# Optimization experiments

Hardware: AMD Instinct MI355X
Metric: run time of the kernel (lower is better)

## Reference

```python
import jax, jax.numpy as jnp
import numpy as np

K = 1024  # num_codebook_vectors
D = 256   # latent_dim


def setup_inputs() -> dict:
    key = jax.random.key(0)
    k1, k2 = jax.random.split(key)
    z = jax.random.normal(k1, (16, D, 64, 64), dtype=jnp.float32)
    # nn.Embedding weight init: uniform(-1/K, 1/K)
    emb_weight = jax.random.uniform(k2, (K, D), dtype=jnp.float32,
                                    minval=-1.0 / K, maxval=1.0 / K)
    return {"z": z, "emb_weight": emb_weight}


def reference(z, emb_weight):
    B, C, H, W = z.shape  # C == D
    # NCHW -> NHWC, flatten to [N, D]
    z_nhwc = jnp.transpose(z, (0, 2, 3, 1))
    zf = z_nhwc.reshape(-1, C)  # [N, D]
    # squared L2 distances: ||z||^2 + ||e||^2 - 2 z e^T
    d = (jnp.sum(zf * zf, axis=1, keepdims=True)
         + jnp.sum(emb_weight * emb_weight, axis=1)
         - 2.0 * jnp.einsum('nd,kd->nk', zf, emb_weight))  # [N, K]
    min_encoding_indices = jnp.argmin(d, axis=1)  # [N] int
    z_q = emb_weight[min_encoding_indices].reshape(B, H, W, C)
    z_q = jnp.transpose(z_q, (0, 3, 1, 2))  # back to NCHW
    return (min_encoding_indices, z_q)
```

## Files before the change

kernel.cpp:

```cpp
#include <hip/hip_runtime.h>
#include <hip/hip_bf16.h>
#include <stdint.h>
#include <stddef.h>

typedef __attribute__((ext_vector_type(4))) float f32x4;
typedef _Float16 f16x8 __attribute__((ext_vector_type(8)));
typedef _Float16 f16x4 __attribute__((ext_vector_type(4)));

#define BN 128
#define MARGIN 230.0f

__device__ float g_embn[1024];

__device__ __forceinline__ int swzA(int n) { return (n ^ (n >> 3)) & 7; }

__global__ __launch_bounds__(256) void emb_prep_kernel(const float* __restrict__ emb,
                                                       _Float16* __restrict__ embf) {
    int row = blockIdx.x * 4 + (threadIdx.x >> 6);
    int l   = threadIdx.x & 63;
    f32x4 v = *(const f32x4*)&emb[(size_t)row * 256 + l * 4];
    f16x4 h;
    float s = 0.f;
#pragma unroll
    for (int j = 0; j < 4; ++j) {
        h[j] = (_Float16)(v[j] * 1024.0f);
        float f = (float)h[j];
        s = fmaf(f, f, s);
    }
    *(f16x4*)&embf[(size_t)row * 256 + l * 4] = h;
#pragma unroll
    for (int off = 1; off < 64; off <<= 1) s += __shfl_xor(s, off, 64);
    if (l == 0) g_embn[row] = s;
}

__device__ __forceinline__ void prefetch_B(const _Float16* __restrict__ embf,
                                           _Float16* bbuf, int s, int t) {
    int kt = s >> 3, ds = s & 7;
    int code = t >> 2;
    int slot = t & 3;
    int g    = (slot ^ code ^ (code >> 2)) & 3;
    const _Float16* src = embf + (((size_t)(kt * 128 + code)) << 8) + ds * 32 + g * 8;
    void* dst = (void*)(bbuf + (size_t)t * 8);
    __builtin_amdgcn_global_load_lds((const __attribute__((address_space(1))) void*)src,
                                     (__attribute__((address_space(3))) void*)dst,
                                     16, 0, 0);
}

__global__ __launch_bounds__(512, 4) void vq_kernel(
        const float* __restrict__ z,
        const float* __restrict__ emb,
        const _Float16* __restrict__ embf,
        float* __restrict__ out) {

    __shared__ _Float16 A_sh[BN * 256];
    __shared__ _Float16 B_sh[2][BN * 32];

    const int t  = threadIdx.x;
    const int w  = t >> 6;
    const int l  = t & 63;
    const int c  = l & 15;
    const int q  = l >> 4;
    const int wr = w >> 1;
    const int wc = w & 1;

    const int n0    = blockIdx.x * BN;
    const int b_img = n0 >> 12;
    const int hw0   = n0 & 4095;
    const float* zb = z + (size_t)b_img * (256 * 4096) + hw0;

    prefetch_B(embf, &B_sh[0][0], 0, t);

#pragma unroll
    for (int it = 0; it < 2; ++it) {
        int task = it * 512 + t;
        int nq = task & 31;
        int dg = task >> 5;
        const float* g = zb + (size_t)(dg * 8) * 4096 + nq * 4;
        f32x4 col[8];
#pragma unroll
        for (int j = 0; j < 8; ++j) col[j] = *(const f32x4*)(g + (size_t)j * 4096);
#pragma unroll
        for (int u = 0; u < 4; ++u) {
            int n = nq * 4 + u;
            f16x8 v;
#pragma unroll
            for (int j = 0; j < 8; ++j) v[j] = (_Float16)col[j][u];
            *(f16x8*)&A_sh[n * 256 + ((dg ^ swzA(n)) * 8)] = v;
        }
    }

    f32x4 acc[2][4];
    float v1[8], v2[8];
    int   i1[8], i2[8];
#pragma unroll
    for (int i = 0; i < 2; ++i)
#pragma unroll
        for (int j = 0; j < 4; ++j) acc[i][j] = (f32x4){0.f, 0.f, 0.f, 0.f};
#pragma unroll
    for (int p = 0; p < 8; ++p) { v1[p] = 3.4e38f; v2[p] = 3.4e38f; i1[p] = 0x7fffffff; i2[p] = 0x7fffffff; }

    for (int kt = 0; kt < 8; ++kt) {
        float en4[4];
#pragma unroll
        for (int j = 0; j < 4; ++j) en4[j] = g_embn[kt * 128 + wc * 64 + j * 16 + c];

#pragma unroll
        for (int ds = 0; ds < 8; ++ds) {
            int s = kt * 8 + ds;
            __syncthreads();
            if (s + 1 < 64) prefetch_B(embf, &B_sh[(s + 1) & 1][0], s + 1, t);

            const _Float16* Bb = &B_sh[s & 1][0];

            f16x8 af[2], bfr[4];
#pragma unroll
            for (int i = 0; i < 2; ++i) {
                int n  = wr * 32 + i * 16 + c;
                int pg = ((ds << 2) + q) ^ swzA(n);
                af[i] = *(const f16x8*)&A_sh[n * 256 + pg * 8];
            }
#pragma unroll
            for (int j = 0; j < 4; ++j) {
                int k = wc * 64 + j * 16 + c;
                bfr[j] = *(const f16x8*)&Bb[k * 32 + (((q ^ k ^ (k >> 2)) & 3) * 8)];
            }
#pragma unroll
            for (int i = 0; i < 2; ++i)
#pragma unroll
                for (int j = 0; j < 4; ++j)
                    acc[i][j] = __builtin_amdgcn_mfma_f32_16x16x32_f16(af[i], bfr[j], acc[i][j], 0, 0, 0);
        }

#pragma unroll
        for (int j = 0; j < 4; ++j) {
            float en = en4[j];
            int code = kt * 128 + wc * 64 + j * 16 + c;
#pragma unroll
            for (int i = 0; i < 2; ++i) {
#pragma unroll
                for (int r = 0; r < 4; ++r) {
                    int p = i * 4 + r;
                    float sc = fmaf(-2048.0f, acc[i][j][r], en);
                    if (sc < v1[p]) {
                        v2[p] = v1[p]; i2[p] = i1[p];
                        v1[p] = sc;    i1[p] = code;
                    } else if (sc < v2[p]) {
                        v2[p] = sc;    i2[p] = code;
                    }
                }
            }
        }
#pragma unroll
        for (int i = 0; i < 2; ++i)
#pragma unroll
            for (int j = 0; j < 4; ++j) acc[i][j] = (f32x4){0.f, 0.f, 0.f, 0.f};
    }

    __syncthreads();

    float* cv = (float*)A_sh;
    int*   ci = ((int*)A_sh) + 8192;
    int* idx_fin = (int*)&B_sh[0][0];
    int* wl_n    = idx_fin + 128;
    int* wl_row  = idx_fin + 129;
    int* wl_nc   = idx_fin + 257;
    int* wl_cand = idx_fin + 385;

    if (t == 0) wl_n[0] = 0;
#pragma unroll
    for (int p = 0; p < 8; ++p) {
        int row = wr * 32 + (p >> 2) * 16 + q * 4 + (p & 3);
        int s0  = (wc * 16 + c) * 2;
        cv[s0 * 128       + ((row + s0)     & 127)] = v1[p];
        ci[s0 * 128       + ((row + s0)     & 127)] = i1[p];
        cv[(s0 + 1) * 128 + ((row + s0 + 1) & 127)] = v2[p];
        ci[(s0 + 1) * 128 + ((row + s0 + 1) & 127)] = i2[p];
    }
    __syncthreads();

    if (t < BN) {
        float mv = 3.4e38f; int mi = 0x7fffffff;
#pragma unroll 8
        for (int s = 0; s < 64; ++s) {
            float v = cv[s * 128 + ((t + s) & 127)];
            int  id = ci[s * 128 + ((t + s) & 127)];
            if (v < mv || (v == mv && id < mi)) { mv = v; mi = id; }
        }
        int   cand[8]; int nc = 0;
        float thr = mv + MARGIN;
        for (int s = 0; s < 64; ++s) {
            float v = cv[s * 128 + ((t + s) & 127)];
            int  id = ci[s * 128 + ((t + s) & 127)];
            if (v <= thr && id < 1024 && nc < 8) cand[nc++] = id;
        }
        idx_fin[t] = mi;
        if (nc > 1) {
            int slot = atomicAdd(wl_n, 1);
            wl_row[slot] = t;
            wl_nc[slot]  = nc;
            for (int i = 0; i < nc; ++i) wl_cand[slot * 8 + i] = cand[i];
        }
    }
    __syncthreads();

    int nwl = wl_n[0];
    for (int e = w; e < nwl; e += 8) {
        int row = wl_row[e];
        int nc  = wl_nc[e];
        const float* zrow = zb + row;

        int j  = l & 15, h = j >> 3, jj = j & 7;
        float x0 = zrow[(size_t)(h * 128 + jj) * 4096];
        float r  = __fmul_rn(x0, x0);
        for (int m = 1; m < 16; ++m) {
            float x = zrow[(size_t)(h * 128 + jj + 8 * m) * 4096];
            r = __fadd_rn(r, __fmul_rn(x, x));
        }
        float s1 = __fadd_rn(r,  __shfl_xor(r,  1, 64));
        float s2 = __fadd_rn(s1, __shfl_xor(s1, 2, 64));
        float s4 = __fadd_rn(s2, __shfl_xor(s2, 4, 64));
        float a_n = __fadd_rn(s4, __shfl_xor(s4, 8, 64));
        a_n = __shfl(a_n, 0, 64);

        float best = 3.4e38f; int bid = 0x7fffffff;
        for (int cx = 0; cx < nc; ++cx) {
            int id = wl_cand[e * 8 + cx];
            const float* er = emb + (size_t)id * 256;
            float y0 = er[h * 128 + jj];
            float rb = __fmul_rn(y0, y0);
            for (int m = 1; m < 16; ++m) {
                float y = er[h * 128 + jj + 8 * m];
                rb = __fadd_rn(rb, __fmul_rn(y, y));
            }
            float b1 = __fadd_rn(rb, __shfl_xor(rb, 1, 64));
            float b2 = __fadd_rn(b1, __shfl_xor(b1, 2, 64));
            float b4 = __fadd_rn(b2, __shfl_xor(b2, 4, 64));
            float b_k = __fadd_rn(b4, __shfl_xor(b4, 8, 64));
            b_k = __shfl(b_k, 0, 64);
            double cd = 0.0;
#pragma unroll
            for (int u = 0; u < 4; ++u) {
                int d = l + u * 64;
                cd = fma((double)zrow[(size_t)d * 4096], (double)er[d], cd);
            }
#pragma unroll
            for (int off = 1; off < 64; off <<= 1) cd += __shfl_xor(cd, off, 64);
            float c32 = (float)cd;
            float sc  = __fsub_rn(__fadd_rn(a_n, b_k), __fmul_rn(2.0f, c32));
            if (sc < best || (sc == best && id < bid)) { best = sc; bid = id; }
        }
        if (l == 0) idx_fin[row] = bid;
    }
    __syncthreads();

    if (t < BN) out[n0 + t] = (float)idx_fin[t];

    float* zq = out + 65536 + (size_t)b_img * (256 * 4096) + hw0;
    {
        int m   = t & 127;
        int sub = t >> 7;
        int id  = idx_fin[m];
        const float* er = emb + (size_t)id * 256;
#pragma unroll 4
        for (int it = 0; it < 16; ++it) {
            int d4 = it * 4 + sub;
            f32x4 v = *(const f32x4*)&er[d4 * 4];
#pragma unroll
            for (int jj2 = 0; jj2 < 4; ++jj2)
                zq[(size_t)(d4 * 4 + jj2) * 4096 + m] = v[jj2];
        }
    }
}

extern "C" void kernel_launch(void* const* d_in, const int* in_sizes, int n_in,
                              void* d_out, int out_size, void* d_ws, size_t ws_size,
                              hipStream_t stream) {
    const float* z   = (const float*)d_in[0];
    const float* emb = (const float*)d_in[1];
    _Float16* embf = (_Float16*)d_ws;
    float* out = (float*)d_out;

    emb_prep_kernel<<<256, 256, 0, stream>>>(emb, embf);
    vq_kernel<<<65536 / BN, 512, 0, stream>>>(z, emb, embf, out);
}
```

Before: 192.0 us.

## Use 1024-thread blocks with 16 waves each computing a 16-row tile

Doubles the block size to 1024 threads so each wave handles 16 rows instead of 32, halving per-wave MFMA work and register state, and spreads the z staging, candidate refinement and gather loops across twice as many threads. The aim is more waves in flight to hide latency. In exchange, each B fragment loaded from LDS now feeds only one A fragment, so LDS read traffic per MFMA rises. The per-step __syncthreads also has to coordinate 16 waves instead of 8.

```diff
diff --git a/kernel.cpp b/kernel.cpp
--- a/kernel.cpp
+++ b/kernel.cpp
@@ -46,7 +46,7 @@
                                      16, 0, 0);
 }
 
-__global__ __launch_bounds__(512, 4) void vq_kernel(
+__global__ __launch_bounds__(1024, 8) void vq_kernel(
         const float* __restrict__ z,
         const float* __restrict__ emb,
         const _Float16* __restrict__ embf,
@@ -68,13 +68,11 @@
     const int hw0   = n0 & 4095;
     const float* zb = z + (size_t)b_img * (256 * 4096) + hw0;
 
-    prefetch_B(embf, &B_sh[0][0], 0, t);
-
-#pragma unroll
-    for (int it = 0; it < 2; ++it) {
-        int task = it * 512 + t;
-        int nq = task & 31;
-        int dg = task >> 5;
+    if (t < 512) prefetch_B(embf, &B_sh[0][0], 0, t);
+
+    {
+        int nq = t & 31;
+        int dg = t >> 5;
         const float* g = zb + (size_t)(dg * 8) * 4096 + nq * 4;
         f32x4 col[8];
 #pragma unroll
@@ -89,15 +87,13 @@
         }
     }
 
-    f32x4 acc[2][4];
-    float v1[8], v2[8];
-    int   i1[8], i2[8];
-#pragma unroll
-    for (int i = 0; i < 2; ++i)
-#pragma unroll
-        for (int j = 0; j < 4; ++j) acc[i][j] = (f32x4){0.f, 0.f, 0.f, 0.f};
-#pragma unroll
-    for (int p = 0; p < 8; ++p) { v1[p] = 3.4e38f; v2[p] = 3.4e38f; i1[p] = 0x7fffffff; i2[p] = 0x7fffffff; }
+    f32x4 acc[4];
+    float v1[4], v2[4];
+    int   i1[4], i2[4];
+#pragma unroll
+    for (int j = 0; j < 4; ++j) acc[j] = (f32x4){0.f, 0.f, 0.f, 0.f};
+#pragma unroll
+    for (int p = 0; p < 4; ++p) { v1[p] = 3.4e38f; v2[p] = 3.4e38f; i1[p] = 0x7fffffff; i2[p] = 0x7fffffff; }
 
     for (int kt = 0; kt < 8; ++kt) {
         float en4[4];
@@ -108,16 +104,15 @@
         for (int ds = 0; ds < 8; ++ds) {
             int s = kt * 8 + ds;
             __syncthreads();
-            if (s + 1 < 64) prefetch_B(embf, &B_sh[(s + 1) & 1][0], s + 1, t);
+            if (s + 1 < 64 && t < 512) prefetch_B(embf, &B_sh[(s + 1) & 1][0], s + 1, t);
 
             const _Float16* Bb = &B_sh[s & 1][0];
 
-            f16x8 af[2], bfr[4];
-#pragma unroll
-            for (int i = 0; i < 2; ++i) {
-                int n  = wr * 32 + i * 16 + c;
+            f16x8 af, bfr[4];
+            {
+                int n  = wr * 16 + c;
                 int pg = ((ds << 2) + q) ^ swzA(n);
-                af[i] = *(const f16x8*)&A_sh[n * 256 + pg * 8];
+                af = *(const f16x8*)&A_sh[n * 256 + pg * 8];
             }
 #pragma unroll
             for (int j = 0; j < 4; ++j) {
@@ -125,10 +120,8 @@
                 bfr[j] = *(const f16x8*)&Bb[k * 32 + (((q ^ k ^ (k >> 2)) & 3) * 8)];
             }
 #pragma unroll
-            for (int i = 0; i < 2; ++i)
-#pragma unroll
-                for (int j = 0; j < 4; ++j)
-                    acc[i][j] = __builtin_amdgcn_mfma_f32_16x16x32_f16(af[i], bfr[j], acc[i][j], 0, 0, 0);
+            for (int j = 0; j < 4; ++j)
+                acc[j] = __builtin_amdgcn_mfma_f32_16x16x32_f16(af, bfr[j], acc[j], 0, 0, 0);
         }
 
 #pragma unroll
@@ -136,24 +129,18 @@
             float en = en4[j];
             int code = kt * 128 + wc * 64 + j * 16 + c;
 #pragma unroll
-            for (int i = 0; i < 2; ++i) {
-#pragma unroll
-                for (int r = 0; r < 4; ++r) {
-                    int p = i * 4 + r;
-                    float sc = fmaf(-2048.0f, acc[i][j][r], en);
-                    if (sc < v1[p]) {
-                        v2[p] = v1[p]; i2[p] = i1[p];
-                        v1[p] = sc;    i1[p] = code;
-                    } else if (sc < v2[p]) {
-                        v2[p] = sc;    i2[p] = code;
-                    }
+            for (int r = 0; r < 4; ++r) {
+                float sc = fmaf(-2048.0f, acc[j][r], en);
+                if (sc < v1[r]) {
+                    v2[r] = v1[r]; i2[r] = i1[r];
+                    v1[r] = sc;    i1[r] = code;
+                } else if (sc < v2[r]) {
+                    v2[r] = sc;    i2[r] = code;
                 }
             }
         }
 #pragma unroll
-        for (int i = 0; i < 2; ++i)
-#pragma unroll
-            for (int j = 0; j < 4; ++j) acc[i][j] = (f32x4){0.f, 0.f, 0.f, 0.f};
+        for (int j = 0; j < 4; ++j) acc[j] = (f32x4){0.f, 0.f, 0.f, 0.f};
     }
 
     __syncthreads();
@@ -168,8 +155,8 @@
 
     if (t == 0) wl_n[0] = 0;
 #pragma unroll
-    for (int p = 0; p < 8; ++p) {
-        int row = wr * 32 + (p >> 2) * 16 + q * 4 + (p & 3);
+    for (int p = 0; p < 4; ++p) {
+        int row = wr * 16 + q * 4 + p;
         int s0  = (wc * 16 + c) * 2;
         cv[s0 * 128       + ((row + s0)     & 127)] = v1[p];
         ci[s0 * 128       + ((row + s0)     & 127)] = i1[p];
@@ -204,7 +191,7 @@
     __syncthreads();
 
     int nwl = wl_n[0];
-    for (int e = w; e < nwl; e += 8) {
+    for (int e = w; e < nwl; e += 16) {
         int row = wl_row[e];
         int nc  = wl_nc[e];
         const float* zrow = zb + row;
@@ -261,9 +248,9 @@
         int sub = t >> 7;
         int id  = idx_fin[m];
         const float* er = emb + (size_t)id * 256;
-#pragma unroll 4
-        for (int it = 0; it < 16; ++it) {
-            int d4 = it * 4 + sub;
+#pragma unroll
+        for (int it = 0; it < 8; ++it) {
+            int d4 = it * 8 + sub;
             f32x4 v = *(const f32x4*)&er[d4 * 4];
 #pragma unroll
             for (int jj2 = 0; jj2 < 4; ++jj2)
@@ -281,5 +268,5 @@
     float* out = (float*)d_out;
 
     emb_prep_kernel<<<256, 256, 0, stream>>>(emb, embf);
-    vq_kernel<<<65536 / BN, 512, 0, stream>>>(z, emb, embf, out);
-}
+    vq_kernel<<<65536 / BN, 1024, 0, stream>>>(z, emb, embf, out);
+}
```

Measured after the change: 220.8 us. 1.15x slower.
